# Kernel tuning notes

Hardware: AMD Instinct MI355X
Metric: run time of the kernel (lower is better)

Reference implementation:

```python
import jax, jax.numpy as jnp
import numpy as np

N = 100000   # vertices
E = 600000   # directed edges
F = 200000   # triangle faces
CIN = 128
COUT = 128
H = 32       # metric MLP hidden
D = 3        # embedding_dim (3D metric)
TRI = D * (D + 1) // 2  # 6 params of a symmetric 3x3


def setup_inputs() -> dict:
    key = jax.random.key(0)
    ks = jax.random.split(key, 8)
    features = jax.random.normal(ks[0], (N, CIN), jnp.float32)
    vertices = jax.random.normal(ks[1], (N, 3), jnp.float32)
    edges = jax.random.randint(ks[2], (2, E), 0, N)
    faces = jax.random.randint(ks[3], (3, F), 0, N)
    # metric MLP params (edge tangent vector -> symmetric metric params)
    W1 = jax.random.normal(ks[4], (D, H), jnp.float32) / np.sqrt(D)
    b1 = jnp.zeros((H,), jnp.float32)
    W2 = jax.random.normal(ks[5], (H, TRI), jnp.float32) / np.sqrt(H)
    b2 = jnp.zeros((TRI,), jnp.float32)
    # per-vertex feature transform
    Wlin = jax.random.normal(ks[6], (CIN, COUT), jnp.float32) / np.sqrt(CIN)
    blin = jnp.zeros((COUT,), jnp.float32)
    return dict(features=features, vertices=vertices, edges=edges, faces=faces,
                W1=W1, b1=b1, W2=W2, b2=b2, Wlin=Wlin, blin=blin)


def _vertex_normals(vertices, faces):
    # area-weighted vertex normals from triangle faces
    v0, v1, v2 = vertices[faces[0]], vertices[faces[1]], vertices[faces[2]]
    fn = jnp.cross(v1 - v0, v2 - v0)                       # [F,3]
    n = jnp.zeros_like(vertices)
    n = n.at[faces[0]].add(fn).at[faces[1]].add(fn).at[faces[2]].add(fn)
    return n / (jnp.linalg.norm(n, axis=-1, keepdims=True) + 1e-8)


def _sym_from_flat(theta):
    # theta [E,6] -> symmetric [E,3,3]
    iu0, iu1 = jnp.triu_indices(D)
    S = jnp.zeros((theta.shape[0], D, D), theta.dtype)
    S = S.at[:, iu0, iu1].set(theta)
    S = S.at[:, iu1, iu0].set(theta)
    return S


def reference(features, vertices, edges, faces, W1, b1, W2, b2, Wlin, blin):
    eps = 1e-5
    src, dst = edges[0], edges[1]
    normals = _vertex_normals(vertices, faces)             # [N,3] ('tangent' info)
    d = vertices[dst] - vertices[src]                      # [E,3] edge vectors
    n_src = normals[src]
    t = d - jnp.sum(d * n_src, -1, keepdims=True) * n_src  # tangent-plane projection
    # learned metric per edge: MLP -> symmetric S, PSD metric M = S S
    h = jax.nn.relu(t @ W1 + b1)                           # [E,H]
    theta = h @ W2 + b2                                    # [E,6]
    S = _sym_from_flat(theta)                              # [E,3,3]
    M = jnp.einsum('eij,ejk->eik', S, S)                   # PSD metric
    q = jnp.einsum('ei,eij,ej->e', t, M, t)                # metric quadratic form
    w = jnp.exp(-q)                                        # positive edge weights
    # per-vertex linear, then metric-weighted mean aggregation over in-edges
    x = features @ Wlin + blin                             # [N,COUT]
    num = jax.ops.segment_sum(w[:, None] * x[src], dst, num_segments=N)
    den = jax.ops.segment_sum(w, dst, num_segments=N) + eps
    out = num / den[:, None]                               # MetricConv output
    # MetricConvBlock: manual per-feature normalization + ELU
    mu = out.mean(axis=0)
    sd = out.std(axis=0, ddof=1)                           # torch std is unbiased
    out = (out - mu) / (sd + eps)
    return jax.nn.elu(out)
```

## Files before the change

### kernel.cpp

```cpp
#include <hip/hip_runtime.h>
#include <hip/hip_bf16.h>
#include <math.h>

#define N_V 100000
#define N_E 600000
#define N_F 200000

typedef __attribute__((ext_vector_type(8))) short bf16x8;
typedef __attribute__((ext_vector_type(4))) float f32x4;

#define FUSED_BLOCKS 782
#define FACE_BLOCKS 782
#define EDGE_BLOCKS 2344
#define PACK_BLOCKS 64
#define CONV_BLOCKS 6250

__device__ __forceinline__ unsigned short f2bf(float f) {
    unsigned int u = __builtin_bit_cast(unsigned int, f);
    u += 0x7fffu + ((u >> 16) & 1u);
    return (unsigned short)(u >> 16);
}
__device__ __forceinline__ float bf2f(short s) {
    return __builtin_bit_cast(float, ((unsigned int)(unsigned short)s) << 16);
}

__global__ void k_fn(const float* __restrict__ vtx, const int* __restrict__ faces,
                     const float* __restrict__ Wlin, const float* __restrict__ feat,
                     float4* __restrict__ fnbuf4,
                     int* __restrict__ head_f, int* __restrict__ next_f,
                     unsigned short* __restrict__ Wb,
                     unsigned short* __restrict__ featb) {
    int b = blockIdx.x;
    int t = threadIdx.x;
    if (b < FACE_BLOCKS) {
        int f = b * 256 + t;
        if (f >= N_F) return;
        int i0 = faces[f], i1 = faces[N_F + f], i2 = faces[2 * N_F + f];
        #pragma unroll
        for (int j = 0; j < 3; j++) {
            int v = (j == 0) ? i0 : (j == 1 ? i1 : i2);
            int c = 3 * f + j;
            int old = atomicExch(&head_f[v], c);
            next_f[c] = old;
        }
        float ax = vtx[3 * i0], ay = vtx[3 * i0 + 1], az = vtx[3 * i0 + 2];
        float bx = vtx[3 * i1] - ax, by = vtx[3 * i1 + 1] - ay, bz = vtx[3 * i1 + 2] - az;
        float cx = vtx[3 * i2] - ax, cy = vtx[3 * i2 + 1] - ay, cz = vtx[3 * i2 + 2] - az;
        float4 fn;
        fn.x = by * cz - bz * cy;
        fn.y = bz * cx - bx * cz;
        fn.z = bx * cy - by * cx;
        fn.w = 0.f;
        fnbuf4[f] = fn;
    } else if (b < FACE_BLOCKS + PACK_BLOCKS) {
        int i = (b - FACE_BLOCKS) * 256 + t;
        int j = i & 7;
        int lane = (i >> 3) & 63;
        int ct = (i >> 9) & 7;
        int kk = i >> 12;
        int k = kk * 32 + (lane >> 4) * 8 + j;
        int n = ct * 16 + (lane & 15);
        Wb[i] = f2bf(Wlin[k * 128 + n]);
    } else {
        int i = (b - FACE_BLOCKS - PACK_BLOCKS) * 256 + t;
        const float4* fp = (const float4*)(feat + (size_t)i * 8);
        float4 f0 = fp[0], f1 = fp[1];
        bf16x8 p;
        p[0] = (short)f2bf(f0.x); p[1] = (short)f2bf(f0.y);
        p[2] = (short)f2bf(f0.z); p[3] = (short)f2bf(f0.w);
        p[4] = (short)f2bf(f1.x); p[5] = (short)f2bf(f1.y);
        p[6] = (short)f2bf(f1.z); p[7] = (short)f2bf(f1.w);
        *(bf16x8*)(featb + (size_t)i * 8) = p;
    }
}

__global__ void k_vnorm(const float4* __restrict__ fnbuf4,
                        const int* __restrict__ head_f, const int* __restrict__ next_f,
                        float4* __restrict__ nrm4) {
    int v = blockIdx.x * 256 + threadIdx.x;
    if (v >= N_V) return;
    float nx = 0.f, ny = 0.f, nz = 0.f;
    int c = head_f[v];
    while (c >= 0) {
        float4 fn = fnbuf4[(unsigned)c / 3u];
        nx += fn.x; ny += fn.y; nz += fn.z;
        c = next_f[c];
    }
    float inv = 1.f / (sqrtf(nx * nx + ny * ny + nz * nz) + 1e-8f);
    float4 o;
    o.x = nx * inv; o.y = ny * inv; o.z = nz * inv; o.w = 0.f;
    nrm4[v] = o;
}

template<int MODE>
__global__ void k_edge_t(const float* __restrict__ vtx, const int* __restrict__ edges,
                         const float4* __restrict__ nrm4,
                         const float* __restrict__ W1, const float* __restrict__ b1,
                         const float* __restrict__ W2, const float* __restrict__ b2,
                         int* __restrict__ head_e, uint2* __restrict__ enode) {
    __shared__ float sW1[96], sb1[32], sW2[192], sb2[6];
    int t = threadIdx.x;
    if (t < 96)  sW1[t] = W1[t];
    if (t < 32)  sb1[t] = b1[t];
    if (t < 192) sW2[t] = W2[t];
    if (t < 6)   sb2[t] = b2[t];
    __syncthreads();
    int e = blockIdx.x * blockDim.x + t;
    if (e >= N_E) return;
    int s = edges[e], d = edges[N_E + e];
    int old = atomicExch(&head_e[d], e);
    float4 nv = nrm4[s];
    float dx = vtx[3 * d] - vtx[3 * s];
    float dy = vtx[3 * d + 1] - vtx[3 * s + 1];
    float dz = vtx[3 * d + 2] - vtx[3 * s + 2];
    float nx = nv.x, ny = nv.y, nz = nv.z;
    float dp = dx * nx + dy * ny + dz * nz;
    float tx = dx - dp * nx, ty = dy - dp * ny, tz = dz - dp * nz;
    float th0 = sb2[0], th1 = sb2[1], th2 = sb2[2], th3 = sb2[3], th4 = sb2[4], th5 = sb2[5];
    #pragma unroll
    for (int j = 0; j < 32; j++) {
        float h = tx * sW1[j] + ty * sW1[32 + j] + tz * sW1[64 + j] + sb1[j];
        h = fmaxf(h, 0.f);
        const float* w2r = &sW2[j * 6];
        th0 += h * w2r[0]; th1 += h * w2r[1]; th2 += h * w2r[2];
        th3 += h * w2r[3]; th4 += h * w2r[4]; th5 += h * w2r[5];
    }
    float ux = th0 * tx + th1 * ty + th2 * tz;
    float uy = th1 * tx + th3 * ty + th4 * tz;
    float uz = th2 * tx + th4 * ty + th5 * tz;
    float q = ux * ux + uy * uy + uz * uz;
    float w = expf(-q);
    unsigned int w16 = f2bf(w);
    uint2 nd;
    if (MODE == 0) {
        nd.x = (unsigned int)(old + 1) | ((w16 & 0xFFFu) << 20);
        nd.y = (unsigned int)s | ((w16 >> 12) << 17);
    } else {
        nd.x = (unsigned int)(old + 1);
        nd.y = (unsigned int)s | (w16 << 17);
    }
    enode[e] = nd;
}

template<int STYLE>
__global__ __launch_bounds__(512) void k_fused_t(const float* __restrict__ feat,
                                                 const unsigned short* __restrict__ featb,
                                                 const int* __restrict__ head_e,
                                                 const uint2* __restrict__ enode,
                                                 const unsigned short* __restrict__ Wb,
                                                 const float* __restrict__ blin,
                                                 float* __restrict__ out,
                                                 float* __restrict__ partials) {
    __shared__ __align__(16) unsigned short At[128 * 136];
    __shared__ float gs[128];
    int t = threadIdx.x;
    int g = t >> 4;
    int gl = t & 15;
    int vb = blockIdx.x * 128 + g * 4;

    float4 a0l = {0,0,0,0}, a0h = {0,0,0,0};
    float4 a1l = {0,0,0,0}, a1h = {0,0,0,0};
    float4 a2l = {0,0,0,0}, a2h = {0,0,0,0};
    float4 a3l = {0,0,0,0}, a3h = {0,0,0,0};
    float d0 = 0.f, d1 = 0.f, d2 = 0.f, d3 = 0.f;
    int e0 = (vb + 0 < N_V) ? head_e[vb + 0] : -1;
    int e1 = (vb + 1 < N_V) ? head_e[vb + 1] : -1;
    int e2 = (vb + 2 < N_V) ? head_e[vb + 2] : -1;
    int e3 = (vb + 3 < N_V) ? head_e[vb + 3] : -1;

#define CHAIN_STEP(eV, aL, aH, dV)                                                   \
    if (eV >= 0) {                                                                   \
        uint2 nd = enode[eV];                                                        \
        unsigned int w16 = (STYLE == 0)                                              \
            ? ((nd.x >> 20) | (((nd.y >> 17) & 0xFu) << 12))                         \
            : (nd.y >> 17);                                                          \
        float w = __builtin_bit_cast(float, w16 << 16);                              \
        unsigned int src = nd.y & 0x1FFFFu;                                          \
        if (STYLE < 2) {                                                             \
            const float4* fp = (const float4*)(feat + (size_t)src * 128 + 8 * gl);   \
            float4 f0 = fp[0], f1 = fp[1];                                           \
            aL.x += w * f0.x; aL.y += w * f0.y; aL.z += w * f0.z; aL.w += w * f0.w;  \
            aH.x += w * f1.x; aH.y += w * f1.y; aH.z += w * f1.z; aH.w += w * f1.w;  \
        } else {                                                                     \
            bf16x8 v = *(const bf16x8*)(featb + (size_t)src * 128 + 8 * gl);         \
            aL.x += w * bf2f(v[0]); aL.y += w * bf2f(v[1]);                          \
            aL.z += w * bf2f(v[2]); aL.w += w * bf2f(v[3]);                          \
            aH.x += w * bf2f(v[4]); aH.y += w * bf2f(v[5]);                          \
            aH.z += w * bf2f(v[6]); aH.w += w * bf2f(v[7]);                          \
        }                                                                            \
        dV += w;                                                                     \
        eV = (int)(nd.x & 0xFFFFFu) - 1;                                             \
    }

    while ((e0 >= 0) || (e1 >= 0) || (e2 >= 0) || (e3 >= 0)) {
        CHAIN_STEP(e0, a0l, a0h, d0)
        CHAIN_STEP(e1, a1l, a1h, d1)
        CHAIN_STEP(e2, a2l, a2h, d2)
        CHAIN_STEP(e3, a3l, a3h, d3)
    }
#undef CHAIN_STEP

    #pragma unroll
    for (int j = 0; j < 4; j++) {
        float4 al = (j == 0) ? a0l : (j == 1) ? a1l : (j == 2) ? a2l : a3l;
        float4 ah = (j == 0) ? a0h : (j == 1) ? a1h : (j == 2) ? a2h : a3h;
        float dn = (j == 0) ? d0 : (j == 1) ? d1 : (j == 2) ? d2 : d3;
        float inv = 1.f / (dn + 1e-5f);
        ushort4 p0, p1;
        p0.x = f2bf(al.x * inv); p0.y = f2bf(al.y * inv);
        p0.z = f2bf(al.z * inv); p0.w = f2bf(al.w * inv);
        p1.x = f2bf(ah.x * inv); p1.y = f2bf(ah.y * inv);
        p1.z = f2bf(ah.z * inv); p1.w = f2bf(ah.w * inv);
        int row = g * 4 + j;
        *(ushort4*)(&At[row * 136 + 8 * gl]) = p0;
        *(ushort4*)(&At[row * 136 + 8 * gl + 4]) = p1;
        if (gl == 0) gs[row] = dn * inv;
    }
    __syncthreads();

    int ct = t >> 6;
    int lane = t & 63;
    int m = lane & 15, quad = lane >> 4;
    bf16x8 bfr[4];
    #pragma unroll
    for (int kk = 0; kk < 4; kk++)
        bfr[kk] = *(const bf16x8*)(Wb + (((kk * 8 + ct) * 64 + lane) << 3));
    float bl = blin[ct * 16 + m];
    float ssr = 0.f, qqr = 0.f;
    #pragma unroll
    for (int tile = 0; tile < 8; tile++) {
        f32x4 acc = (f32x4){0.f, 0.f, 0.f, 0.f};
        #pragma unroll
        for (int kk = 0; kk < 4; kk++) {
            bf16x8 af = *(const bf16x8*)(&At[(tile * 16 + m) * 136 + kk * 32 + quad * 8]);
            acc = __builtin_amdgcn_mfma_f32_16x16x32_bf16(af, bfr[kk], acc, 0, 0, 0);
        }
        int r0 = blockIdx.x * 128 + tile * 16;
        #pragma unroll
        for (int reg = 0; reg < 4; reg++) {
            int r = r0 + quad * 4 + reg;
            float g2 = gs[tile * 16 + quad * 4 + reg];
            float val = acc[reg] + bl * g2;
            if (r < N_V) out[(size_t)r * 128 + ct * 16 + m] = val;
            ssr += val; qqr += val * val;
        }
    }
    ssr += __shfl_xor(ssr, 16); qqr += __shfl_xor(qqr, 16);
    ssr += __shfl_xor(ssr, 32); qqr += __shfl_xor(qqr, 32);
    if (quad == 0) {
        partials[(size_t)blockIdx.x * 256 + ct * 16 + m] = ssr;
        partials[(size_t)blockIdx.x * 256 + 128 + ct * 16 + m] = qqr;
    }
}

__global__ __launch_bounds__(64) void k_rstats(const float* __restrict__ partials,
                                               float* __restrict__ stats) {
    int c = blockIdx.x;
    int lane = threadIdx.x;
    float s = 0.f, q = 0.f;
    for (int b = lane; b < FUSED_BLOCKS; b += 64) {
        s += partials[(size_t)b * 256 + c];
        q += partials[(size_t)b * 256 + 128 + c];
    }
    #pragma unroll
    for (int off = 32; off; off >>= 1) {
        s += __shfl_down(s, off);
        q += __shfl_down(q, off);
    }
    if (lane == 0) {
        float mu = s * (1.f / N_V);
        float var = (q - s * mu) * (1.f / (N_V - 1));
        float sd = sqrtf(fmaxf(var, 0.f));
        stats[c] = mu;
        stats[128 + c] = 1.f / (sd + 1e-5f);
    }
}

__global__ void k_finalize(float* __restrict__ out, const float* __restrict__ stats) {
    int i = blockIdx.x * blockDim.x + threadIdx.x;
    if (i >= N_V * 32) return;
    float4 v = ((float4*)out)[i];
    int c0 = (i * 4) & 127;
    float mu0 = stats[c0], mu1 = stats[c0 + 1], mu2 = stats[c0 + 2], mu3 = stats[c0 + 3];
    float is0 = stats[128 + c0], is1 = stats[128 + c0 + 1], is2 = stats[128 + c0 + 2], is3 = stats[128 + c0 + 3];
    v.x = (v.x - mu0) * is0; v.y = (v.y - mu1) * is1;
    v.z = (v.z - mu2) * is2; v.w = (v.w - mu3) * is3;
    v.x = v.x > 0.f ? v.x : expm1f(v.x);
    v.y = v.y > 0.f ? v.y : expm1f(v.y);
    v.z = v.z > 0.f ? v.z : expm1f(v.z);
    v.w = v.w > 0.f ? v.w : expm1f(v.w);
    ((float4*)out)[i] = v;
}

extern "C" void kernel_launch(void* const* d_in, const int* in_sizes, int n_in,
                              void* d_out, int out_size, void* d_ws, size_t ws_size,
                              hipStream_t stream) {
    const float* feat  = (const float*)d_in[0];
    const float* vtx   = (const float*)d_in[1];
    const int*   edges = (const int*)d_in[2];
    const int*   faces = (const int*)d_in[3];
    const float* W1   = (const float*)d_in[4];
    const float* b1   = (const float*)d_in[5];
    const float* W2   = (const float*)d_in[6];
    const float* b2   = (const float*)d_in[7];
    const float* Wlin = (const float*)d_in[8];
    const float* blin = (const float*)d_in[9];
    float* out = (float*)d_out;
    float* ws = (float*)d_ws;

    int*   head_e   = (int*)ws;
    int*   head_f   = (int*)(ws + 100000);
    float4* nrm4    = (float4*)(ws + 200000);
    float* partials = ws + 100000;
    int*   next_f   = (int*)(ws + 600128);
    float4* fnbuf4  = (float4*)(ws + 1200128);
    uint2* enode    = (uint2*)(ws + 600128);
    unsigned short* Wb = (unsigned short*)(ws + 2000128);
    unsigned short* featb = (unsigned short*)(ws + 2008320);
    float* stats    = ws;

    const size_t NEED2 = 8408320u * 4u;
    int tier2 = (ws_size >= NEED2) ? 1 : 0;

    hipMemsetAsync(head_e, 0xFF, 200000 * sizeof(int), stream);

    int fn_grid = FACE_BLOCKS + PACK_BLOCKS + (tier2 ? CONV_BLOCKS : 0);
    k_fn<<<fn_grid, 256, 0, stream>>>(vtx, faces, Wlin, feat, fnbuf4,
                                      head_f, next_f, Wb, tier2 ? featb : nullptr);
    k_vnorm<<<(N_V + 255) / 256, 256, 0, stream>>>(fnbuf4, head_f, next_f, nrm4);
    if (tier2) {
        k_edge_t<1><<<EDGE_BLOCKS, 256, 0, stream>>>(vtx, edges, nrm4, W1, b1, W2, b2,
                                                     head_e, enode);
        k_fused_t<2><<<FUSED_BLOCKS, 512, 0, stream>>>(feat, featb, head_e, enode, Wb,
                                                       blin, out, partials);
    } else {
        k_edge_t<0><<<EDGE_BLOCKS, 256, 0, stream>>>(vtx, edges, nrm4, W1, b1, W2, b2,
                                                     head_e, enode);
        k_fused_t<0><<<FUSED_BLOCKS, 512, 0, stream>>>(feat, nullptr, head_e, enode, Wb,
                                                       blin, out, partials);
    }
    k_rstats<<<128, 64, 0, stream>>>(partials, stats);
    k_finalize<<<(N_V * 32 + 255) / 256, 256, 0, stream>>>(out, stats);
}
```

Baseline: 253.0 us.

## Fuse vertex-normal gather into edge kernel and merge stats with finalize

On the large-workspace path, the separate vertex-normal kernel is removed. Each edge thread now walks the source vertex's face list and normalizes inline, so the same normals are recomputed for every out-edge (about 6x redundant work) in exchange for one fewer launch and no normal buffer round-trip. The column-stats reduction and the normalize+ELU pass are merged into one grid-stride kernel. Every block redundantly reduces all partials before the elementwise pass, and the workspace layout is rearranged so enode gets its own region.

```diff
diff --git a/kernel.cpp b/kernel.cpp
--- a/kernel.cpp
+++ b/kernel.cpp
@@ -14,6 +14,7 @@
 #define EDGE_BLOCKS 2344
 #define PACK_BLOCKS 64
 #define CONV_BLOCKS 6250
+#define BACK_BLOCKS 512
 
 __device__ __forceinline__ unsigned short f2bf(float f) {
     unsigned int u = __builtin_bit_cast(unsigned int, f);
@@ -92,12 +93,63 @@
     nrm4[v] = o;
 }
 
-template<int MODE>
-__global__ void k_edge_t(const float* __restrict__ vtx, const int* __restrict__ edges,
-                         const float4* __restrict__ nrm4,
-                         const float* __restrict__ W1, const float* __restrict__ b1,
-                         const float* __restrict__ W2, const float* __restrict__ b2,
-                         int* __restrict__ head_e, uint2* __restrict__ enode) {
+__global__ void k_edge2(const float* __restrict__ vtx, const int* __restrict__ edges,
+                        const float4* __restrict__ fnbuf4,
+                        const int* __restrict__ head_f, const int* __restrict__ next_f,
+                        const float* __restrict__ W1, const float* __restrict__ b1,
+                        const float* __restrict__ W2, const float* __restrict__ b2,
+                        int* __restrict__ head_e, uint2* __restrict__ enode) {
+    __shared__ float sW1[96], sb1[32], sW2[192], sb2[6];
+    int t = threadIdx.x;
+    if (t < 96)  sW1[t] = W1[t];
+    if (t < 32)  sb1[t] = b1[t];
+    if (t < 192) sW2[t] = W2[t];
+    if (t < 6)   sb2[t] = b2[t];
+    __syncthreads();
+    int e = blockIdx.x * blockDim.x + t;
+    if (e >= N_E) return;
+    int s = edges[e], d = edges[N_E + e];
+    int old = atomicExch(&head_e[d], e);
+    float nx = 0.f, ny = 0.f, nz = 0.f;
+    int c = head_f[s];
+    while (c >= 0) {
+        float4 fn = fnbuf4[(unsigned)c / 3u];
+        nx += fn.x; ny += fn.y; nz += fn.z;
+        c = next_f[c];
+    }
+    float ninv = 1.f / (sqrtf(nx * nx + ny * ny + nz * nz) + 1e-8f);
+    nx *= ninv; ny *= ninv; nz *= ninv;
+    float dx = vtx[3 * d] - vtx[3 * s];
+    float dy = vtx[3 * d + 1] - vtx[3 * s + 1];
+    float dz = vtx[3 * d + 2] - vtx[3 * s + 2];
+    float dp = dx * nx + dy * ny + dz * nz;
+    float tx = dx - dp * nx, ty = dy - dp * ny, tz = dz - dp * nz;
+    float th0 = sb2[0], th1 = sb2[1], th2 = sb2[2], th3 = sb2[3], th4 = sb2[4], th5 = sb2[5];
+    #pragma unroll
+    for (int j = 0; j < 32; j++) {
+        float h = tx * sW1[j] + ty * sW1[32 + j] + tz * sW1[64 + j] + sb1[j];
+        h = fmaxf(h, 0.f);
+        const float* w2r = &sW2[j * 6];
+        th0 += h * w2r[0]; th1 += h * w2r[1]; th2 += h * w2r[2];
+        th3 += h * w2r[3]; th4 += h * w2r[4]; th5 += h * w2r[5];
+    }
+    float ux = th0 * tx + th1 * ty + th2 * tz;
+    float uy = th1 * tx + th3 * ty + th4 * tz;
+    float uz = th2 * tx + th4 * ty + th5 * tz;
+    float q = ux * ux + uy * uy + uz * uz;
+    float w = expf(-q);
+    unsigned int w16 = f2bf(w);
+    uint2 nd;
+    nd.x = (unsigned int)(old + 1);
+    nd.y = (unsigned int)s | (w16 << 17);
+    enode[e] = nd;
+}
+
+__global__ void k_edge0(const float* __restrict__ vtx, const int* __restrict__ edges,
+                        const float4* __restrict__ nrm4,
+                        const float* __restrict__ W1, const float* __restrict__ b1,
+                        const float* __restrict__ W2, const float* __restrict__ b2,
+                        int* __restrict__ head_e, uint2* __restrict__ enode) {
     __shared__ float sW1[96], sb1[32], sW2[192], sb2[6];
     int t = threadIdx.x;
     if (t < 96)  sW1[t] = W1[t];
@@ -132,13 +184,8 @@
     float w = expf(-q);
     unsigned int w16 = f2bf(w);
     uint2 nd;
-    if (MODE == 0) {
-        nd.x = (unsigned int)(old + 1) | ((w16 & 0xFFFu) << 20);
-        nd.y = (unsigned int)s | ((w16 >> 12) << 17);
-    } else {
-        nd.x = (unsigned int)(old + 1);
-        nd.y = (unsigned int)s | (w16 << 17);
-    }
+    nd.x = (unsigned int)(old + 1) | ((w16 & 0xFFFu) << 20);
+    nd.y = (unsigned int)s | ((w16 >> 12) << 17);
     enode[e] = nd;
 }
 
@@ -253,6 +300,47 @@
     }
 }
 
+__global__ __launch_bounds__(256) void k_back(const float* __restrict__ partials,
+                                              float* __restrict__ out) {
+    __shared__ float smu[128], sis[128];
+    int t = threadIdx.x;
+    float a0 = 0.f, a1 = 0.f, a2 = 0.f, a3 = 0.f;
+    int b = 0;
+    for (; b + 4 <= FUSED_BLOCKS; b += 4) {
+        a0 += partials[(size_t)(b + 0) * 256 + t];
+        a1 += partials[(size_t)(b + 1) * 256 + t];
+        a2 += partials[(size_t)(b + 2) * 256 + t];
+        a3 += partials[(size_t)(b + 3) * 256 + t];
+    }
+    for (; b < FUSED_BLOCKS; b++) a0 += partials[(size_t)b * 256 + t];
+    float acc = (a0 + a1) + (a2 + a3);
+    __shared__ float sstat[256];
+    sstat[t] = acc;
+    __syncthreads();
+    if (t < 128) {
+        float s = sstat[t], q = sstat[128 + t];
+        float mu = s * (1.f / N_V);
+        float var = (q - s * mu) * (1.f / (N_V - 1));
+        float sd = sqrtf(fmaxf(var, 0.f));
+        smu[t] = mu;
+        sis[t] = 1.f / (sd + 1e-5f);
+    }
+    __syncthreads();
+    for (int i = blockIdx.x * 256 + t; i < N_V * 32; i += BACK_BLOCKS * 256) {
+        float4 v = ((float4*)out)[i];
+        int c0 = (i * 4) & 127;
+        float m0 = smu[c0], m1 = smu[c0 + 1], m2 = smu[c0 + 2], m3 = smu[c0 + 3];
+        float i0 = sis[c0], i1 = sis[c0 + 1], i2 = sis[c0 + 2], i3 = sis[c0 + 3];
+        v.x = (v.x - m0) * i0; v.y = (v.y - m1) * i1;
+        v.z = (v.z - m2) * i2; v.w = (v.w - m3) * i3;
+        v.x = v.x > 0.f ? v.x : expm1f(v.x);
+        v.y = v.y > 0.f ? v.y : expm1f(v.y);
+        v.z = v.z > 0.f ? v.z : expm1f(v.z);
+        v.w = v.w > 0.f ? v.w : expm1f(v.w);
+        ((float4*)out)[i] = v;
+    }
+}
+
 __global__ __launch_bounds__(64) void k_rstats(const float* __restrict__ partials,
                                                float* __restrict__ stats) {
     int c = blockIdx.x;
@@ -308,37 +396,47 @@
     float* out = (float*)d_out;
     float* ws = (float*)d_ws;
 
-    int*   head_e   = (int*)ws;
-    int*   head_f   = (int*)(ws + 100000);
-    float4* nrm4    = (float4*)(ws + 200000);
-    float* partials = ws + 100000;
-    int*   next_f   = (int*)(ws + 600128);
-    float4* fnbuf4  = (float4*)(ws + 1200128);
-    uint2* enode    = (uint2*)(ws + 600128);
-    unsigned short* Wb = (unsigned short*)(ws + 2000128);
-    unsigned short* featb = (unsigned short*)(ws + 2008320);
-    float* stats    = ws;
-
-    const size_t NEED2 = 8408320u * 4u;
-    int tier2 = (ws_size >= NEED2) ? 1 : 0;
-
-    hipMemsetAsync(head_e, 0xFF, 200000 * sizeof(int), stream);
-
-    int fn_grid = FACE_BLOCKS + PACK_BLOCKS + (tier2 ? CONV_BLOCKS : 0);
-    k_fn<<<fn_grid, 256, 0, stream>>>(vtx, faces, Wlin, feat, fnbuf4,
-                                      head_f, next_f, Wb, tier2 ? featb : nullptr);
-    k_vnorm<<<(N_V + 255) / 256, 256, 0, stream>>>(fnbuf4, head_f, next_f, nrm4);
-    if (tier2) {
-        k_edge_t<1><<<EDGE_BLOCKS, 256, 0, stream>>>(vtx, edges, nrm4, W1, b1, W2, b2,
-                                                     head_e, enode);
+    const size_t NEED = 9600128u * 4u;
+
+    if (ws_size >= NEED) {
+        int*   head_e   = (int*)ws;
+        int*   head_f   = (int*)(ws + 100000);
+        float* partials = ws + 100000;
+        unsigned short* Wb = (unsigned short*)(ws + 300192);
+        int*   next_f   = (int*)(ws + 600128);
+        float4* fnbuf4  = (float4*)(ws + 1200128);
+        unsigned short* featb = (unsigned short*)(ws + 2000128);
+        uint2* enode    = (uint2*)(ws + 8400128);
+
+        hipMemsetAsync(head_e, 0xFF, 200000 * sizeof(int), stream);
+        k_fn<<<FACE_BLOCKS + PACK_BLOCKS + CONV_BLOCKS, 256, 0, stream>>>(
+            vtx, faces, Wlin, feat, fnbuf4, head_f, next_f, Wb, featb);
+        k_edge2<<<EDGE_BLOCKS, 256, 0, stream>>>(vtx, edges, fnbuf4, head_f, next_f,
+                                                 W1, b1, W2, b2, head_e, enode);
         k_fused_t<2><<<FUSED_BLOCKS, 512, 0, stream>>>(feat, featb, head_e, enode, Wb,
                                                        blin, out, partials);
+        k_back<<<BACK_BLOCKS, 256, 0, stream>>>(partials, out);
     } else {
-        k_edge_t<0><<<EDGE_BLOCKS, 256, 0, stream>>>(vtx, edges, nrm4, W1, b1, W2, b2,
-                                                     head_e, enode);
+        int*   head_e   = (int*)ws;
+        int*   head_f   = (int*)(ws + 100000);
+        float4* nrm4    = (float4*)(ws + 200000);
+        float* partials = ws + 100000;
+        int*   next_f   = (int*)(ws + 600128);
+        float4* fnbuf4  = (float4*)(ws + 1200128);
+        uint2* enode    = (uint2*)(ws + 600128);
+        unsigned short* Wb = (unsigned short*)(ws + 2000128);
+        float* stats    = ws;
+
+        hipMemsetAsync(head_e, 0xFF, 200000 * sizeof(int), stream);
+        k_fn<<<FACE_BLOCKS + PACK_BLOCKS, 256, 0, stream>>>(vtx, faces, Wlin, feat,
+                                                            fnbuf4, head_f, next_f,
+                                                            Wb, nullptr);
+        k_vnorm<<<(N_V + 255) / 256, 256, 0, stream>>>(fnbuf4, head_f, next_f, nrm4);
+        k_edge0<<<EDGE_BLOCKS, 256, 0, stream>>>(vtx, edges, nrm4, W1, b1, W2, b2,
+                                                 head_e, enode);
         k_fused_t<0><<<FUSED_BLOCKS, 512, 0, stream>>>(feat, nullptr, head_e, enode, Wb,
                                                        blin, out, partials);
-    }
-    k_rstats<<<128, 64, 0, stream>>>(partials, stats);
-    k_finalize<<<(N_V * 32 + 255) / 256, 256, 0, stream>>>(out, stats);
-}
+        k_rstats<<<128, 64, 0, stream>>>(partials, stats);
+        k_finalize<<<(N_V * 32 + 255) / 256, 256, 0, stream>>>(out, stats);
+    }
+}
```

New measurement: 299.2 us. 1.18x slower.
